# Kernel tuning notes

Hardware: AMD Instinct MI355X
Metric: run time of the kernel (lower is better)

Reference implementation:

```python
import jax, jax.numpy as jnp
import numpy as np


def _ln(x, g, b, eps=1e-5):
    m = x.mean(-1, keepdims=True)
    v = x.var(-1, keepdims=True)
    return (x - m) / jnp.sqrt(v + eps) * g + b


def setup_inputs() -> dict:
    key = jax.random.key(0)
    ks = jax.random.split(key, 10)
    N, H, E, OUT, L = 4096, 256, 131072, 64, 6
    s = 1.0 / np.sqrt(H)
    return {
        "x": jax.random.normal(ks[0], (N, H), jnp.float32),
        "edge_index": jax.random.randint(ks[1], (2, E), 0, N, jnp.int32),
        "sage_wl": jax.random.normal(ks[2], (L, H, H), jnp.float32) * s,   # lin_l (neighbors, has bias)
        "sage_wr": jax.random.normal(ks[3], (L, H, H), jnp.float32) * s,   # lin_r (root, no bias)
        "sage_bl": jnp.zeros((L, H), jnp.float32),
        "ln_g": jnp.ones((L - 1, H), jnp.float32),
        "ln_b": jnp.zeros((L - 1, H), jnp.float32),
        "conv_w": jax.random.normal(ks[4], (3, H, H, 3), jnp.float32) * (1.0 / np.sqrt(3 * H)),  # [layer,O,I,K]
        "conv_b": jnp.zeros((3, H), jnp.float32),
        "cnorm_g": jnp.ones((3, H), jnp.float32),
        "cnorm_b": jnp.zeros((3, H), jnp.float32),
        "in_proj_w": jax.random.normal(ks[5], (6 * H, 2 * H), jnp.float32) * (1.0 / np.sqrt(2 * H)),
        "in_proj_b": jnp.zeros((6 * H,), jnp.float32),
        "out_proj_w": jax.random.normal(ks[6], (2 * H, 2 * H), jnp.float32) * (1.0 / np.sqrt(2 * H)),
        "out_proj_b": jnp.zeros((2 * H,), jnp.float32),
        "anorm_g": jnp.ones((2 * H,), jnp.float32),
        "anorm_b": jnp.zeros((2 * H,), jnp.float32),
        "fuse_w": jax.random.normal(ks[7], (OUT, 2 * H), jnp.float32) * (1.0 / np.sqrt(2 * H)),
        "fuse_b": jnp.zeros((OUT,), jnp.float32),
    }


def reference(x, edge_index, sage_wl, sage_wr, sage_bl, ln_g, ln_b,
              conv_w, conv_b, cnorm_g, cnorm_b,
              in_proj_w, in_proj_b, out_proj_w, out_proj_b,
              anorm_g, anorm_b, fuse_w, fuse_b):
    # Dropout layers act as identity (eval mode).
    N, H = x.shape
    L = sage_wl.shape[0]
    src, dst = edge_index[0], edge_index[1]
    deg = jax.ops.segment_sum(jnp.ones(src.shape[0], x.dtype), dst, num_segments=N)
    deg = jnp.maximum(deg, 1.0)[:, None]
    h = x
    for i in range(L):
        res = h
        # SAGEConv: mean-aggregate neighbor features (gather/scatter), then two linears
        agg = jax.ops.segment_sum(h[src], dst, num_segments=N) / deg
        h = agg @ sage_wl[i].T + sage_bl[i] + h @ sage_wr[i].T
        if i < L - 1:
            h = _ln(h, ln_g[i], ln_b[i])
        h = jax.nn.relu(h) + res  # residual (shapes always match: in==hidden)
    gnn_out = h                                   # [N, H]

    # CNN branch over the node axis: [1, H, N]
    c = gnn_out.T[None]
    for j in range(3):
        c = jax.lax.conv_general_dilated(c, conv_w[j], (1,), ((1, 1),),
                                         dimension_numbers=("NCH", "OIH", "NCH"))
        c = jax.nn.relu(c + conv_b[j][None, :, None])
        c = _ln(c.transpose(0, 2, 1), cnorm_g[j], cnorm_b[j]).transpose(0, 2, 1)
    cnn_out = c[0].T                              # [N, H]

    fused = jnp.concatenate([gnn_out, cnn_out], axis=1)  # [N, 2H]
    E2 = fused.shape[1]
    heads = 4
    hd = E2 // heads
    qkv = fused @ in_proj_w.T + in_proj_b
    q, k, v = jnp.split(qkv, 3, axis=1)
    split_heads = lambda t: t.reshape(N, heads, hd).transpose(1, 0, 2)  # [h, N, hd]
    q, k, v = split_heads(q), split_heads(k), split_heads(v)
    scores = jnp.einsum("hnd,hmd->hnm", q, k) / np.sqrt(hd).astype(np.float32)
    a = jax.nn.softmax(scores, axis=-1)
    o = jnp.einsum("hnm,hmd->hnd", a, v).transpose(1, 0, 2).reshape(N, E2)
    o = o @ out_proj_w.T + out_proj_b
    o = _ln(o, anorm_g, anorm_b)
    return o @ fuse_w.T + fuse_b                  # [N, out_channels]
```

## Files before the change

kernel.cpp:

```cpp
#include <hip/hip_runtime.h>

#define NN 4096
#define HH 256
#define EE 131072

__device__ __constant__ float LN_EPS = 1e-5f;
#define ATT_SCALE 0.08838834764831845f
#define ATT_SHIFT 30.0f

typedef __attribute__((ext_vector_type(8))) short bf16x8_t;
typedef __attribute__((ext_vector_type(4))) float f32x4_t;

__device__ inline ushort f2b(float f) {
  uint u = __float_as_uint(f);
  uint r = (u + 0x7FFF + ((u >> 16) & 1)) >> 16;
  return (ushort)r;
}
__device__ inline float b2f(ushort u) { return __uint_as_float((uint)u << 16); }

__global__ void hist_kernel(const int* __restrict__ ei, int* __restrict__ cnt) {
  int e = blockIdx.x * blockDim.x + threadIdx.x;
  if (e < EE) atomicAdd(&cnt[ei[EE + e]], 1);
}

__global__ __launch_bounds__(1024) void scan_kernel(int* __restrict__ cnt_cursor,
                                                    int* __restrict__ rowptr,
                                                    float* __restrict__ invdeg) {
  __shared__ int part[1024];
  int t = threadIdx.x;
  int base = t * 4;
  int cs[4];
  int s = 0;
  for (int u = 0; u < 4; ++u) { cs[u] = cnt_cursor[base + u]; s += cs[u]; }
  part[t] = s;
  __syncthreads();
  for (int off = 1; off < 1024; off <<= 1) {
    int add = (t >= off) ? part[t - off] : 0;
    int v = part[t];
    __syncthreads();
    part[t] = v + add;
    __syncthreads();
  }
  int excl = (t > 0) ? part[t - 1] : 0;
  for (int u = 0; u < 4; ++u) {
    rowptr[base + u] = excl;
    cnt_cursor[base + u] = excl;
    invdeg[base + u] = 1.0f / (float)max(cs[u], 1);
    excl += cs[u];
  }
  if (t == 1023) rowptr[NN] = excl;
}

__global__ void fill_kernel(const int* __restrict__ ei, int* __restrict__ cursor,
                            int* __restrict__ col) {
  int e = blockIdx.x * blockDim.x + threadIdx.x;
  if (e < EE) {
    int d = ei[EE + e];
    int p = atomicAdd(&cursor[d], 1);
    col[p] = ei[e];
  }
}

__global__ __launch_bounds__(256) void castall(
    const float* __restrict__ wl, const float* __restrict__ wr,
    const float* __restrict__ cw, const float* __restrict__ ip,
    const float* __restrict__ opw,
    ushort* __restrict__ wlb, ushort* __restrict__ wrb, ushort* __restrict__ cvb,
    ushort* __restrict__ ipb, ushort* __restrict__ opb) {
  int i4 = (blockIdx.x * 256 + threadIdx.x) * 4;
  if (i4 >= 2424832) return;
  ushort4 o;
  if (i4 < 393216) {
    float4 v = *(const float4*)(wl + i4);
    o.x = f2b(v.x); o.y = f2b(v.y); o.z = f2b(v.z); o.w = f2b(v.w);
    *(ushort4*)(wlb + i4) = o;
  } else if (i4 < 786432) {
    int p = i4 - 393216;
    float4 v = *(const float4*)(wr + p);
    o.x = f2b(v.x); o.y = f2b(v.y); o.z = f2b(v.z); o.w = f2b(v.w);
    *(ushort4*)(wrb + p) = o;
  } else if (i4 < 1376256) {
    int p = i4 - 786432;
    ushort tmp[4];
#pragma unroll
    for (int u = 0; u < 4; ++u) {
      int idx = p + u;
      int j = idx / 196608;
      int rem = idx - j * 196608;
      int oc = rem / 768;
      int kk = rem - oc * 768;
      int ks = kk >> 8, ii = kk & 255;
      tmp[u] = f2b(cw[j * 196608 + oc * 768 + ii * 3 + ks]);
    }
    o.x = tmp[0]; o.y = tmp[1]; o.z = tmp[2]; o.w = tmp[3];
    *(ushort4*)(cvb + p) = o;
  } else if (i4 < 2162688) {
    int p = i4 - 1376256;
    float4 v = *(const float4*)(ip + p);
    o.x = f2b(v.x); o.y = f2b(v.y); o.z = f2b(v.z); o.w = f2b(v.w);
    *(ushort4*)(ipb + p) = o;
  } else {
    int p = i4 - 2162688;
    float4 v = *(const float4*)(opw + p);
    o.x = f2b(v.x); o.y = f2b(v.y); o.z = f2b(v.z); o.w = f2b(v.w);
    *(ushort4*)(opb + p) = o;
  }
}

__global__ __launch_bounds__(256) void copycast(const float* __restrict__ x,
                                                float* __restrict__ h,
                                                ushort* __restrict__ hb) {
  int i4 = (blockIdx.x * 256 + threadIdx.x) * 4;
  float4 v = *(const float4*)(x + i4);
  *(float4*)(h + i4) = v;
  ushort4 w;
  w.x = f2b(v.x); w.y = f2b(v.y); w.z = f2b(v.z); w.w = f2b(v.w);
  *(ushort4*)(hb + i4) = w;
}

__global__ __launch_bounds__(64) void agg_kernel(const ushort* __restrict__ hb,
                                                 const int* __restrict__ rowptr,
                                                 const int* __restrict__ col,
                                                 const float* __restrict__ invdeg,
                                                 ushort* __restrict__ aggb) {
  int n = blockIdx.x;
  int t = threadIdx.x;
  int s = rowptr[n], e = rowptr[n + 1];
  float4 acc = make_float4(0.f, 0.f, 0.f, 0.f);
  for (int j = s; j < e; ++j) {
    int c = col[j];
    ushort4 v = *(const ushort4*)(hb + (size_t)c * HH + t * 4);
    acc.x += b2f(v.x); acc.y += b2f(v.y); acc.z += b2f(v.z); acc.w += b2f(v.w);
  }
  float id = invdeg[n];
  ushort4 w;
  w.x = f2b(acc.x * id); w.y = f2b(acc.y * id);
  w.z = f2b(acc.z * id); w.w = f2b(acc.w * id);
  *(ushort4*)(aggb + (size_t)n * HH + t * 4) = w;
}

__global__ __launch_bounds__(256) void gemm_mfma(
    const ushort* __restrict__ A0, const ushort* __restrict__ A1,
    const ushort* __restrict__ B0, const ushort* __restrict__ B1,
    const float* __restrict__ bias, float* __restrict__ Cf, ushort* __restrict__ Cb,
    int M, int Nn, int K, int KHA, int KHB, int relu) {
  __shared__ ushort Alds[64][40];
  __shared__ ushort Blds[128][40];
  int t = threadIdx.x;
  int w = t >> 6, l = t & 63, quad = l >> 4, lr = l & 15;
  int wm = w & 1, wn = w >> 1;
  int m0 = blockIdx.x * 64, n0 = blockIdx.y * 128;
  int sr = t >> 2, sc8 = (t & 3) * 8;
  f32x4_t acc[2][4];
#pragma unroll
  for (int s = 0; s < 2; ++s)
#pragma unroll
    for (int q = 0; q < 4; ++q) acc[s][q] = (f32x4_t){0.f, 0.f, 0.f, 0.f};

  for (int k0 = 0; k0 < K; k0 += 32) {
    int kk = k0 + sc8;
    const ushort* ap = (kk < KHA) ? (A0 + (size_t)(m0 + sr) * KHA + kk)
                                  : (A1 + (size_t)(m0 + sr) * (K - KHA) + (kk - KHA));
    uint4 av = *(const uint4*)ap;
    const ushort* bp0 = (kk < KHB) ? (B0 + (size_t)(n0 + sr) * KHB + kk)
                                   : (B1 + (size_t)(n0 + sr) * (K - KHB) + (kk - KHB));
    uint4 bv0 = *(const uint4*)bp0;
    const ushort* bp1 = (kk < KHB) ? (B0 + (size_t)(n0 + 64 + sr) * KHB + kk)
                                   : (B1 + (size_t)(n0 + 64 + sr) * (K - KHB) + (kk - KHB));
    uint4 bv1 = *(const uint4*)bp1;
    __syncthreads();
    *(uint4*)&Alds[sr][sc8] = av;
    *(uint4*)&Blds[sr][sc8] = bv0;
    *(uint4*)&Blds[64 + sr][sc8] = bv1;
    __syncthreads();
    bf16x8_t af[2], bf[4];
#pragma unroll
    for (int s = 0; s < 2; ++s)
      af[s] = *(const bf16x8_t*)&Alds[wm * 32 + s * 16 + lr][quad * 8];
#pragma unroll
    for (int q = 0; q < 4; ++q)
      bf[q] = *(const bf16x8_t*)&Blds[wn * 64 + q * 16 + lr][quad * 8];
#pragma unroll
    for (int s = 0; s < 2; ++s)
#pragma unroll
      for (int q = 0; q < 4; ++q)
        acc[s][q] = __builtin_amdgcn_mfma_f32_16x16x32_bf16(af[s], bf[q], acc[s][q], 0, 0, 0);
  }
#pragma unroll
  for (int s = 0; s < 2; ++s) {
#pragma unroll
    for (int q = 0; q < 4; ++q) {
      int n = n0 + wn * 64 + q * 16 + lr;
      float bb = bias[n];
#pragma unroll
      for (int r = 0; r < 4; ++r) {
        int m = m0 + wm * 32 + s * 16 + quad * 4 + r;
        float v = acc[s][q][r] + bb;
        if (relu) v = fmaxf(v, 0.f);
        if (Cf) Cf[(size_t)m * Nn + n] = v;
        if (Cb) Cb[(size_t)m * Nn + n] = f2b(v);
      }
    }
  }
}

__global__ __launch_bounds__(256) void gemm_dual(
    const ushort* __restrict__ A0, const ushort* __restrict__ B0,
    const float* __restrict__ bias0, float* __restrict__ C0,
    const ushort* __restrict__ A1, const ushort* __restrict__ B1,
    float* __restrict__ C1) {
  __shared__ ushort Alds[64][40];
  __shared__ ushort Blds[128][40];
  int t = threadIdx.x;
  int w = t >> 6, l = t & 63, quad = l >> 4, lr = l & 15;
  int wm = w & 1, wn = w >> 1;
  int m0 = blockIdx.x * 64, n0 = blockIdx.y * 128;
  int z = blockIdx.z;
  const ushort* A = z ? A1 : A0;
  const ushort* B = z ? B1 : B0;
  float* C = z ? C1 : C0;
  int sr = t >> 2, sc8 = (t & 3) * 8;
  f32x4_t acc[2][4];
#pragma unroll
  for (int s = 0; s < 2; ++s)
#pragma unroll
    for (int q = 0; q < 4; ++q) acc[s][q] = (f32x4_t){0.f, 0.f, 0.f, 0.f};

  for (int k0 = 0; k0 < 256; k0 += 32) {
    int kk = k0 + sc8;
    uint4 av = *(const uint4*)(A + (size_t)(m0 + sr) * 256 + kk);
    uint4 bv0 = *(const uint4*)(B + (size_t)(n0 + sr) * 256 + kk);
    uint4 bv1 = *(const uint4*)(B + (size_t)(n0 + 64 + sr) * 256 + kk);
    __syncthreads();
    *(uint4*)&Alds[sr][sc8] = av;
    *(uint4*)&Blds[sr][sc8] = bv0;
    *(uint4*)&Blds[64 + sr][sc8] = bv1;
    __syncthreads();
    bf16x8_t af[2], bf[4];
#pragma unroll
    for (int s = 0; s < 2; ++s)
      af[s] = *(const bf16x8_t*)&Alds[wm * 32 + s * 16 + lr][quad * 8];
#pragma unroll
    for (int q = 0; q < 4; ++q)
      bf[q] = *(const bf16x8_t*)&Blds[wn * 64 + q * 16 + lr][quad * 8];
#pragma unroll
    for (int s = 0; s < 2; ++s)
#pragma unroll
      for (int q = 0; q < 4; ++q)
        acc[s][q] = __builtin_amdgcn_mfma_f32_16x16x32_bf16(af[s], bf[q], acc[s][q], 0, 0, 0);
  }
#pragma unroll
  for (int s = 0; s < 2; ++s) {
#pragma unroll
    for (int q = 0; q < 4; ++q) {
      int n = n0 + wn * 64 + q * 16 + lr;
      float bb = z ? 0.f : bias0[n];
#pragma unroll
      for (int r = 0; r < 4; ++r) {
        int m = m0 + wm * 32 + s * 16 + quad * 4 + r;
        C[(size_t)m * 256 + n] = acc[s][q][r] + bb;
      }
    }
  }
}

__global__ __launch_bounds__(256) void gemm_conv_mfma(
    const ushort* __restrict__ Ab, const ushort* __restrict__ B,
    const float* __restrict__ bias, float* __restrict__ C0, float* __restrict__ C1) {
  __shared__ ushort Alds[64][40];
  __shared__ ushort Blds[128][40];
  int t = threadIdx.x;
  int w = t >> 6, l = t & 63, quad = l >> 4, lr = l & 15;
  int wm = w & 1, wn = w >> 1;
  int m0 = blockIdx.x * 64, n0 = blockIdx.y * 128;
  int z = blockIdx.z;
  float* C = z ? C1 : C0;
  int sr = t >> 2, sc8 = (t & 3) * 8;
  f32x4_t acc[2][4];
#pragma unroll
  for (int s = 0; s < 2; ++s)
#pragma unroll
    for (int q = 0; q < 4; ++q) acc[s][q] = (f32x4_t){0.f, 0.f, 0.f, 0.f};

  for (int k0 = 0; k0 < 384; k0 += 32) {
    int kk = z * 384 + k0 + sc8;
    int ks = kk >> 8, ii = kk & 255;
    int nr = m0 + sr + ks - 1;
    uint4 av = make_uint4(0u, 0u, 0u, 0u);
    if (nr >= 0 && nr < NN) av = *(const uint4*)(Ab + (size_t)nr * HH + ii);
    uint4 bv0 = *(const uint4*)(B + (size_t)(n0 + sr) * 768 + kk);
    uint4 bv1 = *(const uint4*)(B + (size_t)(n0 + 64 + sr) * 768 + kk);
    __syncthreads();
    *(uint4*)&Alds[sr][sc8] = av;
    *(uint4*)&Blds[sr][sc8] = bv0;
    *(uint4*)&Blds[64 + sr][sc8] = bv1;
    __syncthreads();
    bf16x8_t af[2], bf[4];
#pragma unroll
    for (int s = 0; s < 2; ++s)
      af[s] = *(const bf16x8_t*)&Alds[wm * 32 + s * 16 + lr][quad * 8];
#pragma unroll
    for (int q = 0; q < 4; ++q)
      bf[q] = *(const bf16x8_t*)&Blds[wn * 64 + q * 16 + lr][quad * 8];
#pragma unroll
    for (int s = 0; s < 2; ++s)
#pragma unroll
      for (int q = 0; q < 4; ++q)
        acc[s][q] = __builtin_amdgcn_mfma_f32_16x16x32_bf16(af[s], bf[q], acc[s][q], 0, 0, 0);
  }
#pragma unroll
  for (int s = 0; s < 2; ++s) {
#pragma unroll
    for (int q = 0; q < 4; ++q) {
      int n = n0 + wn * 64 + q * 16 + lr;
      float bb = z ? 0.f : bias[n];
#pragma unroll
      for (int r = 0; r < 4; ++r) {
        int m = m0 + wm * 32 + s * 16 + quad * 4 + r;
        C[(size_t)m * HH + n] = acc[s][q][r] + bb;
      }
    }
  }
}

__global__ __launch_bounds__(256) void gemm_std(
    const float* __restrict__ A0, const float* __restrict__ B0,
    const float* __restrict__ bias, float* __restrict__ C,
    int M, int Nn, int K) {
  __shared__ float As[16][68];
  __shared__ float Bs[16][68];
  int t = threadIdx.x;
  int m0 = blockIdx.x * 64, n0 = blockIdx.y * 64;
  int ty = t >> 4, tx = t & 15;
  int lr = t >> 2, lc4 = (t & 3) * 4;
  float acc[4][4] = {};
  for (int k0 = 0; k0 < K; k0 += 16) {
    int kk = k0 + lc4;
    float4 va = *(const float4*)(A0 + (size_t)(m0 + lr) * K + kk);
    As[lc4 + 0][lr] = va.x; As[lc4 + 1][lr] = va.y;
    As[lc4 + 2][lr] = va.z; As[lc4 + 3][lr] = va.w;
    float4 vb = *(const float4*)(B0 + (size_t)(n0 + lr) * K + kk);
    Bs[lc4 + 0][lr] = vb.x; Bs[lc4 + 1][lr] = vb.y;
    Bs[lc4 + 2][lr] = vb.z; Bs[lc4 + 3][lr] = vb.w;
    __syncthreads();
#pragma unroll
    for (int k = 0; k < 16; ++k) {
      float4 a4 = *(const float4*)&As[k][4 * ty];
      float4 b4 = *(const float4*)&Bs[k][4 * tx];
      float av[4] = {a4.x, a4.y, a4.z, a4.w};
      float bv[4] = {b4.x, b4.y, b4.z, b4.w};
#pragma unroll
      for (int i = 0; i < 4; ++i)
#pragma unroll
        for (int j = 0; j < 4; ++j) acc[i][j] += av[i] * bv[j];
    }
    __syncthreads();
  }
#pragma unroll
  for (int i = 0; i < 4; ++i) {
    int m = m0 + 4 * ty + i;
    float o[4];
#pragma unroll
    for (int j = 0; j < 4; ++j) o[j] = acc[i][j] + bias[n0 + 4 * tx + j];
    float4 o4 = make_float4(o[0], o[1], o[2], o[3]);
    *(float4*)(C + (size_t)m * Nn + n0 + 4 * tx) = o4;
  }
}

__global__ __launch_bounds__(256) void ln_fuse(
    const float* __restrict__ x, const float* __restrict__ x2,
    const float* __restrict__ g, const float* __restrict__ b,
    const float* __restrict__ res, float* __restrict__ outf, ushort* __restrict__ outb,
    int D, int do_ln, int relu_res, int prerelu) {
  int row = blockIdx.x, t = threadIdx.x;
  int nv = D >> 8;
  float vals[2];
  float s = 0.f, sq = 0.f;
  for (int u = 0; u < nv; ++u) {
    int c = t + (u << 8);
    float v = x[(size_t)row * D + c];
    if (x2) v += x2[(size_t)row * D + c];
    if (prerelu) v = fmaxf(v, 0.f);
    vals[u] = v; s += v; sq += v * v;
  }
  __shared__ float red[8];
  float m = 0.f, inv = 1.f;
  if (do_ln) {
    for (int off = 32; off >= 1; off >>= 1) {
      s += __shfl_xor(s, off);
      sq += __shfl_xor(sq, off);
    }
    int wid = t >> 6;
    if ((t & 63) == 0) { red[wid] = s; red[4 + wid] = sq; }
    __syncthreads();
    if (t == 0) {
      float S = red[0] + red[1] + red[2] + red[3];
      float Q = red[4] + red[5] + red[6] + red[7];
      float mm = S / D;
      float vv = Q / D - mm * mm;
      red[0] = mm;
      red[1] = rsqrtf(vv + LN_EPS);
    }
    __syncthreads();
    m = red[0]; inv = red[1];
  }
  for (int u = 0; u < nv; ++u) {
    int c = t + (u << 8);
    float y = vals[u];
    if (do_ln) y = (y - m) * inv * g[c] + b[c];
    if (relu_res) y = fmaxf(y, 0.f) + res[(size_t)row * D + c];
    if (outf) outf[(size_t)row * D + c] = y;
    if (outb) outb[(size_t)row * D + c] = f2b(y);
  }
}

__global__ __launch_bounds__(256) void kvpack(const ushort* __restrict__ qkvb,
                                              ushort* __restrict__ Kt,
                                              ushort* __restrict__ VtT) {
  int t = threadIdx.x;
  int n0 = blockIdx.x * 32;
  int by = blockIdx.y;
  int kt = n0 >> 5;
  {
    int head = by >> 2, ks = by & 3;
    int key = t >> 3, e4 = (t & 7) * 4;
    uint2 v = *(const uint2*)(qkvb + (size_t)(n0 + key) * 1536 + 512 + head * 128 + ks * 32 + e4);
    *(uint2*)(Kt + ((((size_t)head * 128 + kt) * 4 + ks) * 32 + key) * 32 + e4) = v;
  }
  __shared__ ushort tile[32][34];
  int d0 = by * 32;
  int tx = t & 31, ty = t >> 5;
#pragma unroll
  for (int u = 0; u < 4; ++u) {
    int r = ty + 8 * u;
    tile[r][tx] = qkvb[(size_t)(n0 + r) * 1536 + 1024 + d0 + tx];
  }
  __syncthreads();
#pragma unroll
  for (int u = 0; u < 4; ++u) {
    int dg = d0 + ty + 8 * u;
    int head = dg >> 7, dl = dg & 127;
    VtT[((((size_t)head * 128 + kt) * 128 + dl) << 5) + tx] = tile[tx][ty + 8 * u];
  }
}

__global__ __launch_bounds__(256, 2) void attn_mfma(const ushort* __restrict__ qkvb,
                                                    const ushort* __restrict__ Kt,
                                                    const ushort* __restrict__ VtT,
                                                    ushort* __restrict__ Opart,
                                                    float* __restrict__ Dpart) {
  __shared__ __align__(16) char smem[33536];
  int t = threadIdx.x;
  int w = t >> 6, l = t & 63;
  int quad = l >> 4, lr = l & 15;
  int head = blockIdx.y;
  int z = blockIdx.z;
  int q0 = blockIdx.x * 32;

  ushort* Pl = (ushort*)smem + w * 1280;

  bf16x8_t qf[2][4];
#pragma unroll
  for (int s = 0; s < 2; ++s)
#pragma unroll
    for (int ks = 0; ks < 4; ++ks)
      qf[s][ks] = *(const bf16x8_t*)(qkvb + (size_t)(q0 + s * 16 + lr) * 1536 +
                                     head * 128 + ks * 32 + quad * 8);

  f32x4_t of[2][8];
#pragma unroll
  for (int s = 0; s < 2; ++s)
#pragma unroll
    for (int dt = 0; dt < 8; ++dt) of[s][dt] = (f32x4_t){0.f, 0.f, 0.f, 0.f};
  float den[2][4] = {{0.f, 0.f, 0.f, 0.f}, {0.f, 0.f, 0.f, 0.f}};

  const int lnoff = lr * 32 + quad * 8;
  const int tile0 = z * 64 + w * 16;

  for (int tt = 0; tt < 16; ++tt) {
    int kt = tile0 + tt;
    const ushort* kbase = Kt + (((size_t)head * 128 + kt) << 12);
    const ushort* vbase = VtT + (((size_t)head * 128 + kt) << 12);

    bf16x8_t kf[4][2];
#pragma unroll
    for (int ks = 0; ks < 4; ++ks)
#pragma unroll
      for (int ct = 0; ct < 2; ++ct)
        kf[ks][ct] = *(const bf16x8_t*)(kbase + ks * 1024 + ct * 512 + lnoff);
    bf16x8_t vf[8];
#pragma unroll
    for (int dt = 0; dt < 8; ++dt)
      vf[dt] = *(const bf16x8_t*)(vbase + dt * 512 + lnoff);

    f32x4_t sf[2][2];
#pragma unroll
    for (int s = 0; s < 2; ++s)
#pragma unroll
      for (int ct = 0; ct < 2; ++ct) sf[s][ct] = (f32x4_t){0.f, 0.f, 0.f, 0.f};
    __builtin_amdgcn_s_setprio(1);
#pragma unroll
    for (int ks = 0; ks < 4; ++ks)
#pragma unroll
      for (int ct = 0; ct < 2; ++ct)
#pragma unroll
        for (int s = 0; s < 2; ++s)
          sf[s][ct] = __builtin_amdgcn_mfma_f32_16x16x32_bf16(qf[s][ks], kf[ks][ct], sf[s][ct], 0, 0, 0);
    __builtin_amdgcn_s_setprio(0);

#pragma unroll
    for (int s = 0; s < 2; ++s)
#pragma unroll
      for (int ct = 0; ct < 2; ++ct)
#pragma unroll
        for (int r = 0; r < 4; ++r) {
          float e = __expf(sf[s][ct][r] * ATT_SCALE - ATT_SHIFT);
          Pl[(s * 16 + quad * 4 + r) * 40 + ct * 16 + lr] = f2b(e);
          den[s][r] += e;
        }

    __builtin_amdgcn_s_setprio(1);
#pragma unroll
    for (int s = 0; s < 2; ++s) {
      bf16x8_t pf = *(const bf16x8_t*)&Pl[(s * 16 + lr) * 40 + quad * 8];
#pragma unroll
      for (int dt = 0; dt < 8; ++dt)
        of[s][dt] = __builtin_amdgcn_mfma_f32_16x16x32_bf16(pf, vf[dt], of[s][dt], 0, 0, 0);
    }
    __builtin_amdgcn_s_setprio(0);
  }

#pragma unroll
  for (int mask = 1; mask < 16; mask <<= 1)
#pragma unroll
    for (int s = 0; s < 2; ++s)
#pragma unroll
      for (int r = 0; r < 4; ++r) den[s][r] += __shfl_xor(den[s][r], mask);

  __syncthreads();
  float* OS   = (float*)smem;
  float* Dsum = (float*)(smem + 32768);
  if (lr == 0) {
#pragma unroll
    for (int s = 0; s < 2; ++s)
#pragma unroll
      for (int r = 0; r < 4; ++r) Dsum[w * 32 + s * 16 + quad * 4 + r] = den[s][r];
  }
  __syncthreads();
  if (t < 32) {
    float dn = Dsum[t] + Dsum[32 + t] + Dsum[64 + t] + Dsum[96 + t];
    Dpart[((size_t)z * NN + q0 + t) * 4 + head] = dn;
  }
  for (int dc = 0; dc < 2; ++dc) {
#pragma unroll
    for (int s = 0; s < 2; ++s)
#pragma unroll
      for (int d2 = 0; d2 < 4; ++d2) {
        int dt = dc * 4 + d2;
#pragma unroll
        for (int r = 0; r < 4; ++r)
          OS[w * 2048 + (s * 16 + quad * 4 + r) * 64 + d2 * 16 + lr] = of[s][dt][r];
      }
    __syncthreads();
#pragma unroll
    for (int k = 0; k < 8; ++k) {
      int idx = t + k * 256;
      int row = idx >> 6, c2 = idx & 63;
      float o = OS[row * 64 + c2] + OS[2048 + row * 64 + c2] +
                OS[4096 + row * 64 + c2] + OS[6144 + row * 64 + c2];
      Opart[((size_t)z * NN + q0 + row) * 512 + head * 128 + dc * 64 + c2] = f2b(o);
    }
    __syncthreads();
  }
}

__global__ __launch_bounds__(256) void attn_merge(const ushort* __restrict__ Opart,
                                                  const float* __restrict__ Dpart,
                                                  ushort* __restrict__ aob) {
  int i8 = (blockIdx.x * 256 + threadIdx.x) * 8;
  int row = i8 >> 9, colg = i8 & 511;
  int head = colg >> 7;
  float inv = 1.f / (Dpart[(size_t)row * 4 + head] + Dpart[((size_t)NN + row) * 4 + head]);
  const ushort4* p0 = (const ushort4*)(Opart + (size_t)row * 512 + colg);
  const ushort4* p1 = (const ushort4*)(Opart + ((size_t)NN + row) * 512 + colg);
  ushort4 o[2];
#pragma unroll
  for (int u = 0; u < 2; ++u) {
    ushort4 a = p0[u], b = p1[u];
    o[u].x = f2b((b2f(a.x) + b2f(b.x)) * inv);
    o[u].y = f2b((b2f(a.y) + b2f(b.y)) * inv);
    o[u].z = f2b((b2f(a.z) + b2f(b.z)) * inv);
    o[u].w = f2b((b2f(a.w) + b2f(b.w)) * inv);
  }
  *(ushort4*)(aob + (size_t)row * 512 + colg) = o[0];
  *(ushort4*)(aob + (size_t)row * 512 + colg + 4) = o[1];
}

extern "C" void kernel_launch(void* const* d_in, const int* in_sizes, int n_in,
                              void* d_out, int out_size, void* d_ws, size_t ws_size,
                              hipStream_t stream) {
  const float* x          = (const float*)d_in[0];
  const int*   ei         = (const int*)d_in[1];
  const float* sage_wl    = (const float*)d_in[2];
  const float* sage_wr    = (const float*)d_in[3];
  const float* sage_bl    = (const float*)d_in[4];
  const float* ln_g       = (const float*)d_in[5];
  const float* ln_b       = (const float*)d_in[6];
  const float* conv_w     = (const float*)d_in[7];
  const float* conv_b     = (const float*)d_in[8];
  const float* cnorm_g    = (const float*)d_in[9];
  const float* cnorm_b    = (const float*)d_in[10];
  const float* in_proj_w  = (const float*)d_in[11];
  const float* in_proj_b  = (const float*)d_in[12];
  const float* out_proj_w = (const float*)d_in[13];
  const float* out_proj_b = (const float*)d_in[14];
  const float* anorm_g    = (const float*)d_in[15];
  const float* anorm_b    = (const float*)d_in[16];
  const float* fuse_w     = (const float*)d_in[17];
  const float* fuse_b     = (const float*)d_in[18];
  float* out = (float*)d_out;

  char* ws = (char*)d_ws;
  const size_t MB = 1 << 20;
  int*    rowptr = (int*)(ws + 0);
  int*    cnt    = (int*)(ws + 65536);
  int*    col    = (int*)(ws + 131072);
  float*  invdeg = (float*)(ws + 786432);
  float*  Dpart  = (float*)(ws + 802816);
  float*  h    = (float*)(ws + 1 * MB);
  ushort* hb   = (ushort*)(ws + 5 * MB);
  ushort* aggb = (ushort*)(ws + 7 * MB);
  float*  tmp  = (float*)(ws + 9 * MB);
  ushort* c0b  = (ushort*)(ws + 13 * MB);
  ushort* c1b  = (ushort*)(ws + 15 * MB);
  ushort* qkvb = (ushort*)(ws + 17 * MB);
  float*  op   = (float*)(ws + 17 * MB);
  float*  tmp2 = (float*)(ws + 25 * MB);
  ushort* Opart = (ushort*)(ws + 5 * MB);
  ushort* Kt   = (ushort*)(ws + 1 * MB);
  ushort* Vt   = (ushort*)(ws + 29 * MB);
  ushort* aob  = (ushort*)(ws + 33 * MB);
  ushort* wlb  = (ushort*)(ws + 37 * MB);
  ushort* wrb  = (ushort*)(ws + 37 * MB + 786432);
  ushort* cvb  = (ushort*)(ws + 37 * MB + 1572864);
  ushort* ipb  = (ushort*)(ws + 37 * MB + 2752512);
  ushort* opb  = (ushort*)(ws + 37 * MB + 4325376);

  castall<<<2368, 256, 0, stream>>>(sage_wl, sage_wr, conv_w, in_proj_w, out_proj_w,
                                    wlb, wrb, cvb, ipb, opb);

  hipMemsetAsync(cnt, 0, NN * sizeof(int), stream);
  hist_kernel<<<EE / 256, 256, 0, stream>>>(ei, cnt);
  scan_kernel<<<1, 1024, 0, stream>>>(cnt, rowptr, invdeg);
  fill_kernel<<<EE / 256, 256, 0, stream>>>(ei, cnt, col);
  copycast<<<(NN * HH) / 1024, 256, 0, stream>>>(x, h, hb);

  for (int i = 0; i < 6; ++i) {
    agg_kernel<<<NN, 64, 0, stream>>>(hb, rowptr, col, invdeg, aggb);
    gemm_dual<<<dim3(64, 2, 2), 256, 0, stream>>>(
        aggb, wlb + (size_t)i * HH * HH, sage_bl + i * HH, tmp,
        hb, wrb + (size_t)i * HH * HH, tmp2);
    int do_ln = (i < 5) ? 1 : 0;
    const float* gp = do_ln ? (ln_g + i * HH) : ln_g;
    const float* bp = do_ln ? (ln_b + i * HH) : ln_b;
    ln_fuse<<<NN, 256, 0, stream>>>(tmp, tmp2, gp, bp, h, h, hb, HH, do_ln, 1, 0);
  }

  const ushort* cin = hb;
  ushort* couts[3] = {c0b, c1b, c0b};
  for (int j = 0; j < 3; ++j) {
    gemm_conv_mfma<<<dim3(64, 2, 2), 256, 0, stream>>>(
        cin, cvb + (size_t)j * HH * 768, conv_b + j * HH, tmp, tmp2);
    ln_fuse<<<NN, 256, 0, stream>>>(tmp, tmp2, cnorm_g + j * HH, cnorm_b + j * HH,
                                    nullptr, nullptr, couts[j], HH, 1, 0, 1);
    cin = couts[j];
  }

  gemm_mfma<<<dim3(64, 12), 256, 0, stream>>>(
      hb, c0b, ipb, nullptr, in_proj_b, nullptr, qkvb, NN, 1536, 512, 256, 512, 0);
  kvpack<<<dim3(NN / 32, 16), 256, 0, stream>>>(qkvb, Kt, Vt);
  attn_mfma<<<dim3(NN / 32, 4, 2), 256, 0, stream>>>(qkvb, Kt, Vt, Opart, Dpart);
  attn_merge<<<(NN * 512) / 2048, 256, 0, stream>>>(Opart, Dpart, aob);

  gemm_mfma<<<dim3(64, 4), 256, 0, stream>>>(
      aob, nullptr, opb, nullptr, out_proj_b, op, nullptr, NN, 512, 512, 512, 512, 0);
  ln_fuse<<<NN, 256, 0, stream>>>(op, nullptr, anorm_g, anorm_b, nullptr, op, nullptr, 512, 1, 0, 0);
  gemm_std<<<dim3(64, 1), 256, 0, stream>>>(op, fuse_w, fuse_b, out, NN, 64, 512);
}
```

Measured before the change: 504.5 us.

## Restructure attention to split head dims across waves with shared LDS K tiles

The attention kernel now handles 64 queries per block, with each wave owning 16 query rows for QK^T and a 32-wide slice of the head dimension for PV. Previously each wave took a quarter of the keys and partial outputs were reduced through LDS. K tiles are staged cooperatively in double-buffered LDS with a prefetch of the next tile, and the P tile is shared across waves through LDS. This removes the cross-wave output reduction and cuts per-wave V loads and register use, at the cost of two block barriers per key tile. kvpack writes K in a fragment-ready layout to match.

```diff
diff --git a/kernel.cpp b/kernel.cpp
--- a/kernel.cpp
+++ b/kernel.cpp
@@ -298,7 +298,7 @@
     bf16x8_t af[2], bf[4];
 #pragma unroll
     for (int s = 0; s < 2; ++s)
-      af[s] = *(const bf16x8_t*)&Alds[wm * 32 + s * 16 + lr][quad * 8];
+      af[s] = *(const bf16x8_t*)&Alds[s * 16 + wm * 32 + lr][quad * 8];
 #pragma unroll
     for (int q = 0; q < 4; ++q)
       bf[q] = *(const bf16x8_t*)&Blds[wn * 64 + q * 16 + lr][quad * 8];
@@ -423,9 +423,14 @@
   int kt = n0 >> 5;
   {
     int head = by >> 2, ks = by & 3;
-    int key = t >> 3, e4 = (t & 7) * 4;
-    uint2 v = *(const uint2*)(qkvb + (size_t)(n0 + key) * 1536 + 512 + head * 128 + ks * 32 + e4);
-    *(uint2*)(Kt + ((((size_t)head * 128 + kt) * 4 + ks) * 32 + key) * 32 + e4) = v;
+    int key5 = t >> 3;
+    int ct = key5 >> 4, lr = key5 & 15;
+    int e8 = t & 7;
+    int quad = e8 >> 1, h4 = (e8 & 1) * 4;
+    uint2 v = *(const uint2*)(qkvb + (size_t)(n0 + key5) * 1536 + 512 + head * 128 +
+                              ks * 32 + quad * 8 + h4);
+    int l = quad * 16 + lr;
+    *(uint2*)(Kt + (((size_t)head * 128 + kt) << 12) + (ks * 2 + ct) * 512 + l * 8 + h4) = v;
   }
   __shared__ ushort tile[32][34];
   int d0 = by * 32;
@@ -449,129 +454,114 @@
                                                     const ushort* __restrict__ VtT,
                                                     ushort* __restrict__ Opart,
                                                     float* __restrict__ Dpart) {
-  __shared__ __align__(16) char smem[33536];
+  __shared__ __align__(16) char smem[21760];
+  ushort* Kl = (ushort*)smem;
+  ushort* Psh = (ushort*)(smem + 16384);
   int t = threadIdx.x;
   int w = t >> 6, l = t & 63;
   int quad = l >> 4, lr = l & 15;
   int head = blockIdx.y;
   int z = blockIdx.z;
-  int q0 = blockIdx.x * 32;
-
-  ushort* Pl = (ushort*)smem + w * 1280;
-
-  bf16x8_t qf[2][4];
-#pragma unroll
-  for (int s = 0; s < 2; ++s)
+  int q0 = blockIdx.x * 64;
+
+  bf16x8_t qf[4];
+#pragma unroll
+  for (int ks = 0; ks < 4; ++ks)
+    qf[ks] = *(const bf16x8_t*)(qkvb + (size_t)(q0 + w * 16 + lr) * 1536 +
+                                head * 128 + ks * 32 + quad * 8);
+
+  f32x4_t of[4][2];
+#pragma unroll
+  for (int rc = 0; rc < 4; ++rc)
+#pragma unroll
+    for (int u = 0; u < 2; ++u) of[rc][u] = (f32x4_t){0.f, 0.f, 0.f, 0.f};
+  float den[4] = {0.f, 0.f, 0.f, 0.f};
+
+  const size_t hk = (size_t)head * 128;
+  {
+    const ushort* kb = Kt + ((hk + z * 64) << 12) + t * 16;
+    uint4 a0 = *(const uint4*)kb;
+    uint4 a1 = *(const uint4*)(kb + 8);
+    *(uint4*)(Kl + t * 16) = a0;
+    *(uint4*)(Kl + t * 16 + 8) = a1;
+  }
+  __syncthreads();
+  int cur = 0;
+
+  for (int tt = 0; tt < 64; ++tt) {
+    int kt = z * 64 + tt;
+    uint4 k0, k1;
+    if (tt < 63) {
+      const ushort* kb = Kt + ((hk + kt + 1) << 12) + t * 16;
+      k0 = *(const uint4*)kb;
+      k1 = *(const uint4*)(kb + 8);
+    }
+    const ushort* vbase = VtT + ((hk + kt) << 12);
+    bf16x8_t vf[2];
+#pragma unroll
+    for (int u = 0; u < 2; ++u)
+      vf[u] = *(const bf16x8_t*)(vbase + (w * 2 + u) * 512 + lr * 32 + quad * 8);
+
+    f32x4_t sf[2];
+    sf[0] = (f32x4_t){0.f, 0.f, 0.f, 0.f};
+    sf[1] = (f32x4_t){0.f, 0.f, 0.f, 0.f};
+    __builtin_amdgcn_s_setprio(1);
 #pragma unroll
     for (int ks = 0; ks < 4; ++ks)
-      qf[s][ks] = *(const bf16x8_t*)(qkvb + (size_t)(q0 + s * 16 + lr) * 1536 +
-                                     head * 128 + ks * 32 + quad * 8);
-
-  f32x4_t of[2][8];
-#pragma unroll
-  for (int s = 0; s < 2; ++s)
-#pragma unroll
-    for (int dt = 0; dt < 8; ++dt) of[s][dt] = (f32x4_t){0.f, 0.f, 0.f, 0.f};
-  float den[2][4] = {{0.f, 0.f, 0.f, 0.f}, {0.f, 0.f, 0.f, 0.f}};
-
-  const int lnoff = lr * 32 + quad * 8;
-  const int tile0 = z * 64 + w * 16;
-
-  for (int tt = 0; tt < 16; ++tt) {
-    int kt = tile0 + tt;
-    const ushort* kbase = Kt + (((size_t)head * 128 + kt) << 12);
-    const ushort* vbase = VtT + (((size_t)head * 128 + kt) << 12);
-
-    bf16x8_t kf[4][2];
-#pragma unroll
-    for (int ks = 0; ks < 4; ++ks)
-#pragma unroll
-      for (int ct = 0; ct < 2; ++ct)
-        kf[ks][ct] = *(const bf16x8_t*)(kbase + ks * 1024 + ct * 512 + lnoff);
-    bf16x8_t vf[8];
-#pragma unroll
-    for (int dt = 0; dt < 8; ++dt)
-      vf[dt] = *(const bf16x8_t*)(vbase + dt * 512 + lnoff);
-
-    f32x4_t sf[2][2];
-#pragma unroll
-    for (int s = 0; s < 2; ++s)
-#pragma unroll
-      for (int ct = 0; ct < 2; ++ct) sf[s][ct] = (f32x4_t){0.f, 0.f, 0.f, 0.f};
+#pragma unroll
+      for (int ct = 0; ct < 2; ++ct) {
+        bf16x8_t kf = *(const bf16x8_t*)(Kl + cur * 4096 + (ks * 2 + ct) * 512 + l * 8);
+        sf[ct] = __builtin_amdgcn_mfma_f32_16x16x32_bf16(qf[ks], kf, sf[ct], 0, 0, 0);
+      }
+    __builtin_amdgcn_s_setprio(0);
+
+#pragma unroll
+    for (int ct = 0; ct < 2; ++ct)
+#pragma unroll
+      for (int r = 0; r < 4; ++r) {
+        float e = __expf(sf[ct][r] * ATT_SCALE - ATT_SHIFT);
+        Psh[w * 640 + (quad * 4 + r) * 40 + ct * 16 + lr] = f2b(e);
+        den[r] += e;
+      }
+    __syncthreads();
+
     __builtin_amdgcn_s_setprio(1);
 #pragma unroll
-    for (int ks = 0; ks < 4; ++ks)
-#pragma unroll
-      for (int ct = 0; ct < 2; ++ct)
-#pragma unroll
-        for (int s = 0; s < 2; ++s)
-          sf[s][ct] = __builtin_amdgcn_mfma_f32_16x16x32_bf16(qf[s][ks], kf[ks][ct], sf[s][ct], 0, 0, 0);
+    for (int rc = 0; rc < 4; ++rc) {
+      bf16x8_t pf = *(const bf16x8_t*)(Psh + rc * 640 + lr * 40 + quad * 8);
+#pragma unroll
+      for (int u = 0; u < 2; ++u)
+        of[rc][u] = __builtin_amdgcn_mfma_f32_16x16x32_bf16(pf, vf[u], of[rc][u], 0, 0, 0);
+    }
     __builtin_amdgcn_s_setprio(0);
 
-#pragma unroll
-    for (int s = 0; s < 2; ++s)
-#pragma unroll
-      for (int ct = 0; ct < 2; ++ct)
-#pragma unroll
-        for (int r = 0; r < 4; ++r) {
-          float e = __expf(sf[s][ct][r] * ATT_SCALE - ATT_SHIFT);
-          Pl[(s * 16 + quad * 4 + r) * 40 + ct * 16 + lr] = f2b(e);
-          den[s][r] += e;
-        }
-
-    __builtin_amdgcn_s_setprio(1);
-#pragma unroll
-    for (int s = 0; s < 2; ++s) {
-      bf16x8_t pf = *(const bf16x8_t*)&Pl[(s * 16 + lr) * 40 + quad * 8];
-#pragma unroll
-      for (int dt = 0; dt < 8; ++dt)
-        of[s][dt] = __builtin_amdgcn_mfma_f32_16x16x32_bf16(pf, vf[dt], of[s][dt], 0, 0, 0);
-    }
-    __builtin_amdgcn_s_setprio(0);
+    if (tt < 63) {
+      *(uint4*)(Kl + (cur ^ 1) * 4096 + t * 16) = k0;
+      *(uint4*)(Kl + (cur ^ 1) * 4096 + t * 16 + 8) = k1;
+    }
+    __syncthreads();
+    cur ^= 1;
   }
 
 #pragma unroll
   for (int mask = 1; mask < 16; mask <<= 1)
 #pragma unroll
-    for (int s = 0; s < 2; ++s)
-#pragma unroll
-      for (int r = 0; r < 4; ++r) den[s][r] += __shfl_xor(den[s][r], mask);
-
-  __syncthreads();
-  float* OS   = (float*)smem;
-  float* Dsum = (float*)(smem + 32768);
+    for (int r = 0; r < 4; ++r) den[r] += __shfl_xor(den[r], mask);
   if (lr == 0) {
 #pragma unroll
-    for (int s = 0; s < 2; ++s)
-#pragma unroll
-      for (int r = 0; r < 4; ++r) Dsum[w * 32 + s * 16 + quad * 4 + r] = den[s][r];
-  }
-  __syncthreads();
-  if (t < 32) {
-    float dn = Dsum[t] + Dsum[32 + t] + Dsum[64 + t] + Dsum[96 + t];
-    Dpart[((size_t)z * NN + q0 + t) * 4 + head] = dn;
-  }
-  for (int dc = 0; dc < 2; ++dc) {
-#pragma unroll
-    for (int s = 0; s < 2; ++s)
-#pragma unroll
-      for (int d2 = 0; d2 < 4; ++d2) {
-        int dt = dc * 4 + d2;
-#pragma unroll
-        for (int r = 0; r < 4; ++r)
-          OS[w * 2048 + (s * 16 + quad * 4 + r) * 64 + d2 * 16 + lr] = of[s][dt][r];
+    for (int r = 0; r < 4; ++r)
+      Dpart[((size_t)z * NN + q0 + w * 16 + quad * 4 + r) * 4 + head] = den[r];
+  }
+#pragma unroll
+  for (int rc = 0; rc < 4; ++rc)
+#pragma unroll
+    for (int u = 0; u < 2; ++u)
+#pragma unroll
+      for (int r = 0; r < 4; ++r) {
+        int row = q0 + rc * 16 + quad * 4 + r;
+        int colg = head * 128 + w * 32 + u * 16 + lr;
+        Opart[((size_t)z * NN + row) * 512 + colg] = f2b(of[rc][u][r]);
       }
-    __syncthreads();
-#pragma unroll
-    for (int k = 0; k < 8; ++k) {
-      int idx = t + k * 256;
-      int row = idx >> 6, c2 = idx & 63;
-      float o = OS[row * 64 + c2] + OS[2048 + row * 64 + c2] +
-                OS[4096 + row * 64 + c2] + OS[6144 + row * 64 + c2];
-      Opart[((size_t)z * NN + q0 + row) * 512 + head * 128 + dc * 64 + c2] = f2b(o);
-    }
-    __syncthreads();
-  }
 }
 
 __global__ __launch_bounds__(256) void attn_merge(const ushort* __restrict__ Opart,
@@ -679,7 +669,7 @@
   gemm_mfma<<<dim3(64, 12), 256, 0, stream>>>(
       hb, c0b, ipb, nullptr, in_proj_b, nullptr, qkvb, NN, 1536, 512, 256, 512, 0);
   kvpack<<<dim3(NN / 32, 16), 256, 0, stream>>>(qkvb, Kt, Vt);
-  attn_mfma<<<dim3(NN / 32, 4, 2), 256, 0, stream>>>(qkvb, Kt, Vt, Opart, Dpart);
+  attn_mfma<<<dim3(NN / 64, 4, 2), 256, 0, stream>>>(qkvb, Kt, Vt, Opart, Dpart);
   attn_merge<<<(NN * 512) / 2048, 256, 0, stream>>>(Opart, Dpart, aob);
 
   gemm_mfma<<<dim3(64, 4), 256, 0, stream>>>(
```

New measurement: 491.1 us. 1.03x faster.
